# Performance work log

Measured on AMD Instinct MI355X. Metric: run time of the kernel, lower is better.

## Reference

```python
import jax, jax.numpy as jnp
import numpy as np

D_MODEL = 4096
D_FF = 11008

def _dequant_matmul(x, w_int, s):
    # x: [N, in], w_int: [out, in] int, s: [out, 1] -> [N, out]
    w = w_int.astype(jnp.float32) * s  # dequantized weight [out, in]
    return x @ w.T

def setup_inputs() -> dict:
    key = jax.random.key(0)
    ks = jax.random.split(key, 7)
    x = jax.random.normal(ks[0], (4, 2048, D_MODEL), dtype=jnp.float32)
    gate_w = jax.random.randint(ks[1], (D_FF, D_MODEL), -128, 128, dtype=jnp.int32)
    up_w = jax.random.randint(ks[2], (D_FF, D_MODEL), -128, 128, dtype=jnp.int32)
    down_w = jax.random.randint(ks[3], (D_MODEL, D_FF), -128, 128, dtype=jnp.int32)
    gate_s = jax.random.uniform(ks[4], (D_FF, 1), dtype=jnp.float32) * 0.01
    up_s = jax.random.uniform(ks[5], (D_FF, 1), dtype=jnp.float32) * 0.01
    down_s = jax.random.uniform(ks[6], (D_MODEL, 1), dtype=jnp.float32) * 0.01
    return {"x": x, "gate_w": gate_w, "gate_s": gate_s, "up_w": up_w,
            "up_s": up_s, "down_w": down_w, "down_s": down_s}

def reference(x, gate_w, gate_s, up_w, up_s, down_w, down_s):
    batch, seq_len, hidden = x.shape
    x_flat = x.reshape(-1, hidden).astype(jnp.float32)
    gate = _dequant_matmul(x_flat, gate_w, gate_s)
    up = _dequant_matmul(x_flat, up_w, up_s)
    h = jax.nn.silu(gate) * up
    out = _dequant_matmul(h, down_w, down_s)
    return out.astype(x.dtype).reshape(batch, seq_len, hidden)
```

## Files before the change

kernel.cpp:

```cpp
#include <hip/hip_runtime.h>


typedef __attribute__((ext_vector_type(8))) __bf16 bf16x8;
typedef __attribute__((ext_vector_type(4))) float f32x4;
typedef __attribute__((ext_vector_type(8))) unsigned short ushort8;
typedef __attribute__((ext_vector_type(4))) int i32x4;

#define D_MODEL 4096
#define D_FF    11008
#define NTOK    8192

static __device__ __forceinline__ unsigned short f32_to_bf16(float f) {
    union { float f; unsigned u; } v; v.f = f;
    unsigned r = v.u + 0x7fffu + ((v.u >> 16) & 1u);
    return (unsigned short)(r >> 16);
}
static __device__ __forceinline__ void gload_lds16(const void* g, void* l) {
    __builtin_amdgcn_global_load_lds(
        (const __attribute__((address_space(1))) void*)g,
        (__attribute__((address_space(3))) void*)l, 16, 0, 0);
}

__global__ __launch_bounds__(256)
void pack_gu_kernel(const int* __restrict__ gw, const int* __restrict__ uw,
                    signed char* __restrict__ out)
{
    long long i = ((long long)blockIdx.x * 256 + threadIdx.x) * 8;
    const int r = (int)(i >> 12);
    const int k = (int)(i & 4095);
    const int src_row = ((r >> 5) << 4) + (r & 15);
    const int* src = ((r >> 4) & 1) ? uw : gw;
    const int* p = src + (size_t)src_row * D_MODEL + k;
    int4 w0 = *(const int4*)(p);
    int4 w1 = *(const int4*)(p + 4);
    union { signed char c[8]; unsigned long long u; } rr;
    rr.c[0] = (signed char)w0.x; rr.c[1] = (signed char)w0.y;
    rr.c[2] = (signed char)w0.z; rr.c[3] = (signed char)w0.w;
    rr.c[4] = (signed char)w1.x; rr.c[5] = (signed char)w1.y;
    rr.c[6] = (signed char)w1.z; rr.c[7] = (signed char)w1.w;
    *(unsigned long long*)(out + i) = rr.u;
}

__global__ __launch_bounds__(256)
void dequant_w_kernel(const int* __restrict__ w, const float* __restrict__ s,
                      unsigned short* __restrict__ out, int cols, long long total)
{
    long long i = ((long long)blockIdx.x * 256 + threadIdx.x) * 8;
    if (i >= total) return;
    float sc = s[(int)(i / cols)];
    int4 w0 = *(const int4*)(w + i);
    int4 w1 = *(const int4*)(w + i + 4);
    ushort8 r;
    r[0] = f32_to_bf16((float)w0.x * sc);
    r[1] = f32_to_bf16((float)w0.y * sc);
    r[2] = f32_to_bf16((float)w0.z * sc);
    r[3] = f32_to_bf16((float)w0.w * sc);
    r[4] = f32_to_bf16((float)w1.x * sc);
    r[5] = f32_to_bf16((float)w1.y * sc);
    r[6] = f32_to_bf16((float)w1.z * sc);
    r[7] = f32_to_bf16((float)w1.w * sc);
    *(ushort8*)(out + i) = r;
}

__global__ __launch_bounds__(256)
void quant_x_kernel(const float* __restrict__ x, signed char* __restrict__ xq,
                    float* __restrict__ xs)
{
    __shared__ float red[4];
    const int row = blockIdx.x;
    const int t   = threadIdx.x;
    const float* xr = x + (size_t)row * D_MODEL;
    float4 v0 = *(const float4*)(xr + t * 16);
    float4 v1 = *(const float4*)(xr + t * 16 + 4);
    float4 v2 = *(const float4*)(xr + t * 16 + 8);
    float4 v3 = *(const float4*)(xr + t * 16 + 12);
    float m = fabsf(v0.x);
    m = fmaxf(m, fabsf(v0.y)); m = fmaxf(m, fabsf(v0.z)); m = fmaxf(m, fabsf(v0.w));
    m = fmaxf(m, fabsf(v1.x)); m = fmaxf(m, fabsf(v1.y)); m = fmaxf(m, fabsf(v1.z)); m = fmaxf(m, fabsf(v1.w));
    m = fmaxf(m, fabsf(v2.x)); m = fmaxf(m, fabsf(v2.y)); m = fmaxf(m, fabsf(v2.z)); m = fmaxf(m, fabsf(v2.w));
    m = fmaxf(m, fabsf(v3.x)); m = fmaxf(m, fabsf(v3.y)); m = fmaxf(m, fabsf(v3.z)); m = fmaxf(m, fabsf(v3.w));
    #pragma unroll
    for (int o = 32; o > 0; o >>= 1) m = fmaxf(m, __shfl_xor(m, o));
    if ((t & 63) == 0) red[t >> 6] = m;
    __syncthreads();
    m = fmaxf(fmaxf(red[0], red[1]), fmaxf(red[2], red[3]));
    m = fmaxf(m, 1e-20f);
    const float inv = 127.0f / m;
    if (t == 0) xs[row] = m / 127.0f;
    union { signed char c[16]; int4 i; } r;
    #pragma unroll
    for (int j = 0; j < 4; ++j) {
        float4 v = (j == 0) ? v0 : (j == 1) ? v1 : (j == 2) ? v2 : v3;
        r.c[j*4+0] = (signed char)(int)rintf(fminf(fmaxf(v.x*inv,-127.f),127.f));
        r.c[j*4+1] = (signed char)(int)rintf(fminf(fmaxf(v.y*inv,-127.f),127.f));
        r.c[j*4+2] = (signed char)(int)rintf(fminf(fmaxf(v.z*inv,-127.f),127.f));
        r.c[j*4+3] = (signed char)(int)rintf(fminf(fmaxf(v.w*inv,-127.f),127.f));
    }
    *(int4*)(xq + (size_t)row * D_MODEL + t * 16) = r.i;
}

__global__ __launch_bounds__(512, 2)
void gemm_i8gu(const signed char* __restrict__ A,
               const signed char* __restrict__ B,
               unsigned short* __restrict__ H,
               const float* __restrict__ xs,
               const float* __restrict__ gs,
               const float* __restrict__ us,
               int M, int NH, int K)
{
    extern __shared__ char smem[];
    const int tid = threadIdx.x;
    const int l   = tid & 63;
    const int w   = tid >> 6;
    const int wm  = w >> 2;
    const int wn  = w & 3;

    const int nbx  = gridDim.x;
    const int nwg  = nbx * gridDim.y;
    const int orig = blockIdx.y * nbx + blockIdx.x;
    const int cpx  = nwg >> 3;
    const int swz  = (orig & 7) * cpx + (orig >> 3);
    const int bn = swz % nbx, bm = swz / nbx;
    const int m0 = bm * 256, n0 = bn * 256;

    const int st_r = tid >> 2;
    const int st_c = ((tid & 3) ^ ((st_r >> 1) & 3)) << 4;
    const signed char* gA = A + (size_t)(m0 + st_r) * K + st_c;
    const signed char* gB = B + (size_t)(n0 + st_r) * K + st_c;
    const size_t ld128 = (size_t)128 * K;

    const int s4v = l >> 4;
    const int rA = wm * 128 + (l & 15);
    const int rB = wn * 64  + (l & 15);
    const int offA = rA * 64 + ((s4v << 4) ^ (((rA >> 1) & 3) << 4));
    const int offB = 16384 + rB * 64 + ((s4v << 4) ^ (((rB >> 1) & 3) << 4));

    i32x4 acc[8][4] = {};
    i32x4 af[4], bfr[4];

#define SBAR()  __builtin_amdgcn_sched_barrier(0)
#define BAR()   __builtin_amdgcn_s_barrier()
#define VM4()   asm volatile("s_waitcnt vmcnt(4)" ::: "memory")

#define ST_A8(SS, NXT) do { \
    const signed char* p_ = gA + ((size_t)(SS) << 6); \
    gload_lds16(p_,         smem + (NXT) + (w << 10)); \
    gload_lds16(p_ + ld128, smem + (NXT) + 8192 + (w << 10)); } while (0)
#define ST_B8(SS, NXT) do { \
    const signed char* p_ = gB + ((size_t)(SS) << 6); \
    gload_lds16(p_,         smem + (NXT) + 16384 + (w << 10)); \
    gload_lds16(p_ + ld128, smem + (NXT) + 16384 + 8192 + (w << 10)); } while (0)

#define MFMA16_I8(MB) do { \
    _Pragma("unroll") \
    for (int mi_ = 0; mi_ < 4; ++mi_) { \
        _Pragma("unroll") \
        for (int ni_ = 0; ni_ < 4; ++ni_) { \
            acc[(MB) + mi_][ni_] = __builtin_amdgcn_mfma_i32_16x16x64_i8( \
                af[mi_], bfr[ni_], acc[(MB) + mi_][ni_], 0, 0, 0); \
        } } } while (0)

#define STEP8(CUR, NXT, SS) do { \
    af[0]  = *(const i32x4*)(smem + (CUR) + offA); \
    af[1]  = *(const i32x4*)(smem + (CUR) + offA + 1024); \
    af[2]  = *(const i32x4*)(smem + (CUR) + offA + 2048); \
    af[3]  = *(const i32x4*)(smem + (CUR) + offA + 3072); \
    bfr[0] = *(const i32x4*)(smem + (CUR) + offB); \
    bfr[1] = *(const i32x4*)(smem + (CUR) + offB + 1024); \
    bfr[2] = *(const i32x4*)(smem + (CUR) + offB + 2048); \
    bfr[3] = *(const i32x4*)(smem + (CUR) + offB + 3072); \
    ST_A8(SS, NXT); \
    SBAR(); BAR(); \
    __builtin_amdgcn_s_setprio(1); MFMA16_I8(0); __builtin_amdgcn_s_setprio(0); \
    SBAR(); BAR(); \
    af[0] = *(const i32x4*)(smem + (CUR) + offA + 4096); \
    af[1] = *(const i32x4*)(smem + (CUR) + offA + 5120); \
    af[2] = *(const i32x4*)(smem + (CUR) + offA + 6144); \
    af[3] = *(const i32x4*)(smem + (CUR) + offA + 7168); \
    ST_B8(SS, NXT); \
    SBAR(); BAR(); \
    __builtin_amdgcn_s_setprio(1); MFMA16_I8(4); __builtin_amdgcn_s_setprio(0); \
    VM4(); SBAR(); BAR(); \
} while (0)

    ST_A8(0, 0);      ST_B8(0, 0);
    ST_A8(1, 32768);  ST_B8(1, 32768);
    VM4(); SBAR(); BAR();

    const int T = K >> 6;
    #pragma unroll 1
    for (int s = 0; s < T; s += 4) {
        int s2 = s + 2; if (s2 >= T) s2 -= T;
        int s3 = s + 3; if (s3 >= T) s3 -= T;
        int s4 = s + 4; if (s4 >= T) s4 -= T;
        int s5 = s + 5; if (s5 >= T) s5 -= T;
        STEP8(0,     65536, s2);
        STEP8(32768, 98304, s3);
        STEP8(65536, 0,     s4);
        STEP8(98304, 32768, s5);
    }
    asm volatile("s_waitcnt vmcnt(0)" ::: "memory");

    const int er = (l >> 4) * 4;
    const int ec = l & 15;
    const int hbase = (n0 >> 1) + wn * 32;
    #pragma unroll
    for (int mi = 0; mi < 8; ++mi) {
        const int rowb = m0 + wm * 128 + mi * 16 + er;
        const float4 xsv = *(const float4*)(xs + rowb);
        #pragma unroll
        for (int p = 0; p < 2; ++p) {
            const int c = hbase + p * 16 + ec;
            const float sg = gs[c];
            const float su = us[c];
            #pragma unroll
            for (int q = 0; q < 4; ++q) {
                const float xsc = (q == 0) ? xsv.x : (q == 1) ? xsv.y
                                 : (q == 2) ? xsv.z : xsv.w;
                float g = (float)acc[mi][2*p][q]     * sg * xsc;
                float u = (float)acc[mi][2*p + 1][q] * su * xsc;
                float sig = 1.0f / (1.0f + __expf(-g));
                H[(size_t)(rowb + q) * NH + c] = f32_to_bf16(g * sig * u);
            }
        }
    }
#undef STEP8
#undef MFMA16_I8
#undef ST_A8
#undef ST_B8
#undef VM4
#undef BAR
#undef SBAR
}

__global__ __launch_bounds__(512, 2)
void gemm256_down(const unsigned short* __restrict__ A,
                  const unsigned short* __restrict__ B,
                  float* __restrict__ C,
                  int M, int N, int K)
{
    extern __shared__ char smem[];
    const int tid = threadIdx.x;
    const int l   = tid & 63;
    const int w   = tid >> 6;
    const int wm  = w >> 2;
    const int wn  = w & 3;

    const int nbx  = gridDim.x;
    const int nwg  = nbx * gridDim.y;
    const int orig = blockIdx.y * nbx + blockIdx.x;
    const int cpx  = nwg >> 3;
    const int swz  = (orig & 7) * cpx + (orig >> 3);
    const int bn = swz % nbx, bm = swz / nbx;
    const int m0 = bm * 256, n0 = bn * 256;

    const int st_r = w * 16 + (l >> 2);
    const int st_c = (((l & 3) ^ ((l >> 3) & 3)) << 3);
    const unsigned short* gA = A + (size_t)(m0 + st_r) * K + st_c;
    const unsigned short* gB = B + (size_t)(n0 + st_r) * K + st_c;
    const size_t ld128 = (size_t)128 * K;

    const int s4v = l >> 4;
    const int rA = wm * 128 + (l & 15);
    const int rB = wn * 64  + (l & 15);
    const int offA = rA * 64 + ((s4v << 4) ^ (((rA >> 1) & 3) << 4));
    const int offB = 32768 + rB * 64 + ((s4v << 4) ^ (((rB >> 1) & 3) << 4));

    f32x4 acc[8][4] = {};
    bf16x8 af[4], bfr[4];

#define SBAR()  __builtin_amdgcn_sched_barrier(0)
#define BAR()   __builtin_amdgcn_s_barrier()
#define VM4()   asm volatile("s_waitcnt vmcnt(4)" ::: "memory")
#define STAGE2(SRC, LOFF) do { \
    gload_lds16((SRC), smem + (LOFF) + (w << 10)); \
    gload_lds16((SRC) + ld128, smem + (LOFF) + 8192 + (w << 10)); } while (0)

#define MFMA16(MB) do { \
    _Pragma("unroll") \
    for (int mi_ = 0; mi_ < 4; ++mi_) { \
        _Pragma("unroll") \
        for (int ni_ = 0; ni_ < 4; ++ni_) { \
            acc[(MB) + mi_][ni_] = __builtin_amdgcn_mfma_f32_16x16x32_bf16( \
                af[mi_], bfr[ni_], acc[(MB) + mi_][ni_], 0, 0, 0); \
        } } } while (0)

#define TILE(DB, KTN) do { \
    const int CB = (DB) * 65536; \
    const int PB = ((DB) ^ 1) * 65536; \
    const unsigned short* sA = gA + ((size_t)(KTN) << 6); \
    const unsigned short* sB = gB + ((size_t)(KTN) << 6); \
    af[0]  = *(const bf16x8*)(smem + CB + offA); \
    af[1]  = *(const bf16x8*)(smem + CB + offA + 1024); \
    af[2]  = *(const bf16x8*)(smem + CB + offA + 2048); \
    af[3]  = *(const bf16x8*)(smem + CB + offA + 3072); \
    bfr[0] = *(const bf16x8*)(smem + CB + offB); \
    bfr[1] = *(const bf16x8*)(smem + CB + offB + 1024); \
    bfr[2] = *(const bf16x8*)(smem + CB + offB + 2048); \
    bfr[3] = *(const bf16x8*)(smem + CB + offB + 3072); \
    STAGE2(sA, PB); \
    SBAR(); BAR(); \
    __builtin_amdgcn_s_setprio(1); MFMA16(0); __builtin_amdgcn_s_setprio(0); \
    SBAR(); BAR(); \
    af[0] = *(const bf16x8*)(smem + CB + offA + 4096); \
    af[1] = *(const bf16x8*)(smem + CB + offA + 5120); \
    af[2] = *(const bf16x8*)(smem + CB + offA + 6144); \
    af[3] = *(const bf16x8*)(smem + CB + offA + 7168); \
    STAGE2(sB, PB + 32768); \
    SBAR(); BAR(); \
    __builtin_amdgcn_s_setprio(1); MFMA16(4); __builtin_amdgcn_s_setprio(0); \
    VM4(); SBAR(); BAR(); \
    af[0]  = *(const bf16x8*)(smem + CB + 16384 + offA); \
    af[1]  = *(const bf16x8*)(smem + CB + 16384 + offA + 1024); \
    af[2]  = *(const bf16x8*)(smem + CB + 16384 + offA + 2048); \
    af[3]  = *(const bf16x8*)(smem + CB + 16384 + offA + 3072); \
    bfr[0] = *(const bf16x8*)(smem + CB + 16384 + offB); \
    bfr[1] = *(const bf16x8*)(smem + CB + 16384 + offB + 1024); \
    bfr[2] = *(const bf16x8*)(smem + CB + 16384 + offB + 2048); \
    bfr[3] = *(const bf16x8*)(smem + CB + 16384 + offB + 3072); \
    STAGE2(sA + 32, PB + 16384); \
    SBAR(); BAR(); \
    __builtin_amdgcn_s_setprio(1); MFMA16(0); __builtin_amdgcn_s_setprio(0); \
    SBAR(); BAR(); \
    af[0] = *(const bf16x8*)(smem + CB + 16384 + offA + 4096); \
    af[1] = *(const bf16x8*)(smem + CB + 16384 + offA + 5120); \
    af[2] = *(const bf16x8*)(smem + CB + 16384 + offA + 6144); \
    af[3] = *(const bf16x8*)(smem + CB + 16384 + offA + 7168); \
    STAGE2(sB + 32, PB + 49152); \
    SBAR(); BAR(); \
    __builtin_amdgcn_s_setprio(1); MFMA16(4); __builtin_amdgcn_s_setprio(0); \
    VM4(); SBAR(); BAR(); \
} while (0)

    STAGE2(gA,      0);
    STAGE2(gB,      32768);
    STAGE2(gA + 32, 16384);
    STAGE2(gB + 32, 49152);
    VM4(); SBAR(); BAR();

    const int T = K >> 6;
    const int T2 = T >> 1;
    #pragma unroll 1
    for (int it = 0; it < T2; ++it) {
        const int t0 = it << 1;
        TILE(0, t0 + 1);
        const int kt2 = (t0 + 2 == T) ? 0 : (t0 + 2);
        TILE(1, kt2);
    }
    asm volatile("s_waitcnt vmcnt(0)" ::: "memory");

    const int er = (l >> 4) * 4;
    const int ec = l & 15;
    #pragma unroll
    for (int mi = 0; mi < 8; ++mi) {
        #pragma unroll
        for (int ni = 0; ni < 4; ++ni) {
            #pragma unroll
            for (int q = 0; q < 4; ++q) {
                int row = m0 + wm * 128 + mi * 16 + er + q;
                int col = n0 + wn * 64  + ni * 16 + ec;
                C[(size_t)row * N + col] = acc[mi][ni][q];
            }
        }
    }
#undef TILE
#undef MFMA16
#undef STAGE2
#undef VM4
#undef BAR
#undef SBAR
}

extern "C" void kernel_launch(void* const* d_in, const int* in_sizes, int n_in,
                              void* d_out, int out_size, void* d_ws, size_t ws_size,
                              hipStream_t stream)
{
    const float* x  = (const float*)d_in[0];
    const int*   gw = (const int*)  d_in[1];
    const float* gs = (const float*)d_in[2];
    const int*   uw = (const int*)  d_in[3];
    const float* us = (const float*)d_in[4];
    const int*   dw = (const int*)  d_in[5];
    const float* dsc= (const float*)d_in[6];

    char* ws = (char*)d_ws;
    signed char*    Xq   = (signed char*)ws;    ws += (size_t)NTOK * D_MODEL;
    float*          xs   = (float*)ws;          ws += (size_t)NTOK * 4;
    signed char*    Wgu8 = (signed char*)ws;    ws += (size_t)2 * D_FF * D_MODEL;
    unsigned short* Wd   = (unsigned short*)ws; ws += (size_t)D_MODEL * D_FF * 2;
    unsigned short* H    = (unsigned short*)ws;

    const long long wtot  = (long long)D_FF * D_MODEL;
    const long long gutot = 2LL * wtot;

    hipFuncSetAttribute(reinterpret_cast<const void*>(gemm_i8gu),
                        hipFuncAttributeMaxDynamicSharedMemorySize, 131072);
    hipFuncSetAttribute(reinterpret_cast<const void*>(gemm256_down),
                        hipFuncAttributeMaxDynamicSharedMemorySize, 131072);

    pack_gu_kernel  <<<(int)(gutot / 2048), 256, 0, stream>>>(gw, uw, Wgu8);
    dequant_w_kernel<<<(int)(wtot  / 2048), 256, 0, stream>>>(dw, dsc, Wd, D_FF, wtot);
    quant_x_kernel  <<<NTOK, 256, 0, stream>>>(x, Xq, xs);

    dim3 g1(2 * D_FF / 256, NTOK / 256);
    gemm_i8gu<<<g1, 512, 131072, stream>>>(Xq, Wgu8, H, xs, gs, us,
                                           NTOK, D_FF, D_MODEL);

    dim3 g3(D_MODEL / 256, NTOK / 256);
    gemm256_down<<<g3, 512, 131072, stream>>>(H, Wd, (float*)d_out,
                                              NTOK, D_MODEL, D_FF);
}
```

Before: 1.539 ms.

## Switch both GEMMs from 16x16 to 32x32 MFMA instructions

Replaces the 16x16x64 int8 and 16x16x32 bf16 MFMA tiles with 32x32x32 int8 and 32x32x16 bf16 instructions in the gate/up and down GEMMs. LDS fragment loads, accumulator layout and epilogue indexing are reworked to match. The gate/up weight interleave in the pack kernel moves from 16-row to 32-row groups so each 32-wide N fragment holds only gate or only up. The intent is fewer MFMA issues and fewer LDS fragment reads per k-step, which raises arithmetic intensity per LDS read. The risk is different register pressure and epilogue store patterns.

```diff
diff --git a/kernel.cpp b/kernel.cpp
--- a/kernel.cpp
+++ b/kernel.cpp
@@ -3,8 +3,10 @@
 
 typedef __attribute__((ext_vector_type(8))) __bf16 bf16x8;
 typedef __attribute__((ext_vector_type(4))) float f32x4;
+typedef __attribute__((ext_vector_type(16))) float f32x16;
 typedef __attribute__((ext_vector_type(8))) unsigned short ushort8;
 typedef __attribute__((ext_vector_type(4))) int i32x4;
+typedef __attribute__((ext_vector_type(16))) int i32x16;
 
 #define D_MODEL 4096
 #define D_FF    11008
@@ -28,8 +30,8 @@
     long long i = ((long long)blockIdx.x * 256 + threadIdx.x) * 8;
     const int r = (int)(i >> 12);
     const int k = (int)(i & 4095);
-    const int src_row = ((r >> 5) << 4) + (r & 15);
-    const int* src = ((r >> 4) & 1) ? uw : gw;
+    const int src_row = ((r >> 6) << 5) + (r & 31);
+    const int* src = ((r >> 5) & 1) ? uw : gw;
     const int* p = src + (size_t)src_row * D_MODEL + k;
     int4 w0 = *(const int4*)(p);
     int4 w1 = *(const int4*)(p + 4);
@@ -129,14 +131,15 @@
     const signed char* gB = B + (size_t)(n0 + st_r) * K + st_c;
     const size_t ld128 = (size_t)128 * K;
 
-    const int s4v = l >> 4;
-    const int rA = wm * 128 + (l & 15);
-    const int rB = wn * 64  + (l & 15);
-    const int offA = rA * 64 + ((s4v << 4) ^ (((rA >> 1) & 3) << 4));
-    const int offB = 16384 + rB * 64 + ((s4v << 4) ^ (((rB >> 1) & 3) << 4));
-
-    i32x4 acc[8][4] = {};
-    i32x4 af[4], bfr[4];
+    const int lc = l & 31;
+    const int lh = l >> 5;
+    const int rA = wm * 128 + lc;
+    const int rB = wn * 64  + lc;
+    const int offA = rA * 64 + ((lh << 4) ^ (((rA >> 1) & 3) << 4));
+    const int offB = 16384 + rB * 64 + ((lh << 4) ^ (((rB >> 1) & 3) << 4));
+
+    i32x16 acc[4][2] = {};
+    i32x4 af[4], bfr[2];
 
 #define SBAR()  __builtin_amdgcn_sched_barrier(0)
 #define BAR()   __builtin_amdgcn_s_barrier()
@@ -151,35 +154,33 @@
     gload_lds16(p_,         smem + (NXT) + 16384 + (w << 10)); \
     gload_lds16(p_ + ld128, smem + (NXT) + 16384 + 8192 + (w << 10)); } while (0)
 
-#define MFMA16_I8(MB) do { \
+#define MFMA8_I8() do { \
     _Pragma("unroll") \
-    for (int mi_ = 0; mi_ < 4; ++mi_) { \
+    for (int mf_ = 0; mf_ < 4; ++mf_) { \
         _Pragma("unroll") \
-        for (int ni_ = 0; ni_ < 4; ++ni_) { \
-            acc[(MB) + mi_][ni_] = __builtin_amdgcn_mfma_i32_16x16x64_i8( \
-                af[mi_], bfr[ni_], acc[(MB) + mi_][ni_], 0, 0, 0); \
+        for (int nf_ = 0; nf_ < 2; ++nf_) { \
+            acc[mf_][nf_] = __builtin_amdgcn_mfma_i32_32x32x32_i8( \
+                af[mf_], bfr[nf_], acc[mf_][nf_], 0, 0, 0); \
         } } } while (0)
 
+#define LOADFRAGS(CUR, KS) do { \
+    af[0]  = *(const i32x4*)(smem + (CUR) + (offA ^ (KS))); \
+    af[1]  = *(const i32x4*)(smem + (CUR) + ((offA + 2048) ^ (KS))); \
+    af[2]  = *(const i32x4*)(smem + (CUR) + ((offA + 4096) ^ (KS))); \
+    af[3]  = *(const i32x4*)(smem + (CUR) + ((offA + 6144) ^ (KS))); \
+    bfr[0] = *(const i32x4*)(smem + (CUR) + (offB ^ (KS))); \
+    bfr[1] = *(const i32x4*)(smem + (CUR) + ((offB + 2048) ^ (KS))); } while (0)
+
 #define STEP8(CUR, NXT, SS) do { \
-    af[0]  = *(const i32x4*)(smem + (CUR) + offA); \
-    af[1]  = *(const i32x4*)(smem + (CUR) + offA + 1024); \
-    af[2]  = *(const i32x4*)(smem + (CUR) + offA + 2048); \
-    af[3]  = *(const i32x4*)(smem + (CUR) + offA + 3072); \
-    bfr[0] = *(const i32x4*)(smem + (CUR) + offB); \
-    bfr[1] = *(const i32x4*)(smem + (CUR) + offB + 1024); \
-    bfr[2] = *(const i32x4*)(smem + (CUR) + offB + 2048); \
-    bfr[3] = *(const i32x4*)(smem + (CUR) + offB + 3072); \
+    LOADFRAGS(CUR, 0); \
     ST_A8(SS, NXT); \
     SBAR(); BAR(); \
-    __builtin_amdgcn_s_setprio(1); MFMA16_I8(0); __builtin_amdgcn_s_setprio(0); \
-    SBAR(); BAR(); \
-    af[0] = *(const i32x4*)(smem + (CUR) + offA + 4096); \
-    af[1] = *(const i32x4*)(smem + (CUR) + offA + 5120); \
-    af[2] = *(const i32x4*)(smem + (CUR) + offA + 6144); \
-    af[3] = *(const i32x4*)(smem + (CUR) + offA + 7168); \
+    __builtin_amdgcn_s_setprio(1); MFMA8_I8(); __builtin_amdgcn_s_setprio(0); \
+    SBAR(); BAR(); \
+    LOADFRAGS(CUR, 32); \
     ST_B8(SS, NXT); \
     SBAR(); BAR(); \
-    __builtin_amdgcn_s_setprio(1); MFMA16_I8(4); __builtin_amdgcn_s_setprio(0); \
+    __builtin_amdgcn_s_setprio(1); MFMA8_I8(); __builtin_amdgcn_s_setprio(0); \
     VM4(); SBAR(); BAR(); \
 } while (0)
 
@@ -201,31 +202,33 @@
     }
     asm volatile("s_waitcnt vmcnt(0)" ::: "memory");
 
-    const int er = (l >> 4) * 4;
-    const int ec = l & 15;
-    const int hbase = (n0 >> 1) + wn * 32;
-    #pragma unroll
-    for (int mi = 0; mi < 8; ++mi) {
-        const int rowb = m0 + wm * 128 + mi * 16 + er;
-        const float4 xsv = *(const float4*)(xs + rowb);
+    {
+        const int c = (n0 >> 1) + wn * 32 + lc;
+        const float sg = gs[c];
+        const float su = us[c];
         #pragma unroll
-        for (int p = 0; p < 2; ++p) {
-            const int c = hbase + p * 16 + ec;
-            const float sg = gs[c];
-            const float su = us[c];
+        for (int mf = 0; mf < 4; ++mf) {
+            const int rb = m0 + wm * 128 + mf * 32 + 4 * lh;
             #pragma unroll
-            for (int q = 0; q < 4; ++q) {
-                const float xsc = (q == 0) ? xsv.x : (q == 1) ? xsv.y
-                                 : (q == 2) ? xsv.z : xsv.w;
-                float g = (float)acc[mi][2*p][q]     * sg * xsc;
-                float u = (float)acc[mi][2*p + 1][q] * su * xsc;
-                float sig = 1.0f / (1.0f + __expf(-g));
-                H[(size_t)(rowb + q) * NH + c] = f32_to_bf16(g * sig * u);
+            for (int q2 = 0; q2 < 4; ++q2) {
+                const float4 xsv = *(const float4*)(xs + rb + 8 * q2);
+                #pragma unroll
+                for (int q = 0; q < 4; ++q) {
+                    const int reg = q2 * 4 + q;
+                    const int row = rb + 8 * q2 + q;
+                    const float xsc = (q == 0) ? xsv.x : (q == 1) ? xsv.y
+                                     : (q == 2) ? xsv.z : xsv.w;
+                    float g = (float)acc[mf][0][reg] * sg * xsc;
+                    float u = (float)acc[mf][1][reg] * su * xsc;
+                    float sig = 1.0f / (1.0f + __expf(-g));
+                    H[(size_t)row * NH + c] = f32_to_bf16(g * sig * u);
+                }
             }
         }
     }
 #undef STEP8
-#undef MFMA16_I8
+#undef LOADFRAGS
+#undef MFMA8_I8
 #undef ST_A8
 #undef ST_B8
 #undef VM4
@@ -260,14 +263,15 @@
     const unsigned short* gB = B + (size_t)(n0 + st_r) * K + st_c;
     const size_t ld128 = (size_t)128 * K;
 
-    const int s4v = l >> 4;
-    const int rA = wm * 128 + (l & 15);
-    const int rB = wn * 64  + (l & 15);
-    const int offA = rA * 64 + ((s4v << 4) ^ (((rA >> 1) & 3) << 4));
-    const int offB = 32768 + rB * 64 + ((s4v << 4) ^ (((rB >> 1) & 3) << 4));
-
-    f32x4 acc[8][4] = {};
-    bf16x8 af[4], bfr[4];
+    const int lc = l & 31;
+    const int lh = l >> 5;
+    const int rA = wm * 128 + lc;
+    const int rB = wn * 64  + lc;
+    const int offA = rA * 64 + ((lh << 4) ^ (((rA >> 1) & 3) << 4));
+    const int offB = 32768 + rB * 64 + ((lh << 4) ^ (((rB >> 1) & 3) << 4));
+
+    f32x16 acc[4][2] = {};
+    bf16x8 af[4], bfr[2];
 
 #define SBAR()  __builtin_amdgcn_sched_barrier(0)
 #define BAR()   __builtin_amdgcn_s_barrier()
@@ -276,59 +280,51 @@
     gload_lds16((SRC), smem + (LOFF) + (w << 10)); \
     gload_lds16((SRC) + ld128, smem + (LOFF) + 8192 + (w << 10)); } while (0)
 
-#define MFMA16(MB) do { \
+#define MFMA8_BF() do { \
     _Pragma("unroll") \
-    for (int mi_ = 0; mi_ < 4; ++mi_) { \
+    for (int mf_ = 0; mf_ < 4; ++mf_) { \
         _Pragma("unroll") \
-        for (int ni_ = 0; ni_ < 4; ++ni_) { \
-            acc[(MB) + mi_][ni_] = __builtin_amdgcn_mfma_f32_16x16x32_bf16( \
-                af[mi_], bfr[ni_], acc[(MB) + mi_][ni_], 0, 0, 0); \
+        for (int nf_ = 0; nf_ < 2; ++nf_) { \
+            acc[mf_][nf_] = __builtin_amdgcn_mfma_f32_32x32x16_bf16( \
+                af[mf_], bfr[nf_], acc[mf_][nf_], 0, 0, 0); \
         } } } while (0)
+
+#define LOADFRAGS(CB, HB, KS) do { \
+    af[0]  = *(const bf16x8*)(smem + (CB) + (HB) + (offA ^ (KS))); \
+    af[1]  = *(const bf16x8*)(smem + (CB) + (HB) + ((offA + 2048) ^ (KS))); \
+    af[2]  = *(const bf16x8*)(smem + (CB) + (HB) + ((offA + 4096) ^ (KS))); \
+    af[3]  = *(const bf16x8*)(smem + (CB) + (HB) + ((offA + 6144) ^ (KS))); \
+    bfr[0] = *(const bf16x8*)(smem + (CB) + (HB) + (offB ^ (KS))); \
+    bfr[1] = *(const bf16x8*)(smem + (CB) + (HB) + ((offB + 2048) ^ (KS))); } while (0)
 
 #define TILE(DB, KTN) do { \
     const int CB = (DB) * 65536; \
     const int PB = ((DB) ^ 1) * 65536; \
     const unsigned short* sA = gA + ((size_t)(KTN) << 6); \
     const unsigned short* sB = gB + ((size_t)(KTN) << 6); \
-    af[0]  = *(const bf16x8*)(smem + CB + offA); \
-    af[1]  = *(const bf16x8*)(smem + CB + offA + 1024); \
-    af[2]  = *(const bf16x8*)(smem + CB + offA + 2048); \
-    af[3]  = *(const bf16x8*)(smem + CB + offA + 3072); \
-    bfr[0] = *(const bf16x8*)(smem + CB + offB); \
-    bfr[1] = *(const bf16x8*)(smem + CB + offB + 1024); \
-    bfr[2] = *(const bf16x8*)(smem + CB + offB + 2048); \
-    bfr[3] = *(const bf16x8*)(smem + CB + offB + 3072); \
+     \
+    LOADFRAGS(CB, 0, 0); \
     STAGE2(sA, PB); \
     SBAR(); BAR(); \
-    __builtin_amdgcn_s_setprio(1); MFMA16(0); __builtin_amdgcn_s_setprio(0); \
-    SBAR(); BAR(); \
-    af[0] = *(const bf16x8*)(smem + CB + offA + 4096); \
-    af[1] = *(const bf16x8*)(smem + CB + offA + 5120); \
-    af[2] = *(const bf16x8*)(smem + CB + offA + 6144); \
-    af[3] = *(const bf16x8*)(smem + CB + offA + 7168); \
+    __builtin_amdgcn_s_setprio(1); MFMA8_BF(); __builtin_amdgcn_s_setprio(0); \
+    SBAR(); BAR(); \
+     \
+    LOADFRAGS(CB, 0, 32); \
     STAGE2(sB, PB + 32768); \
     SBAR(); BAR(); \
-    __builtin_amdgcn_s_setprio(1); MFMA16(4); __builtin_amdgcn_s_setprio(0); \
+    __builtin_amdgcn_s_setprio(1); MFMA8_BF(); __builtin_amdgcn_s_setprio(0); \
     VM4(); SBAR(); BAR(); \
-    af[0]  = *(const bf16x8*)(smem + CB + 16384 + offA); \
-    af[1]  = *(const bf16x8*)(smem + CB + 16384 + offA + 1024); \
-    af[2]  = *(const bf16x8*)(smem + CB + 16384 + offA + 2048); \
-    af[3]  = *(const bf16x8*)(smem + CB + 16384 + offA + 3072); \
-    bfr[0] = *(const bf16x8*)(smem + CB + 16384 + offB); \
-    bfr[1] = *(const bf16x8*)(smem + CB + 16384 + offB + 1024); \
-    bfr[2] = *(const bf16x8*)(smem + CB + 16384 + offB + 2048); \
-    bfr[3] = *(const bf16x8*)(smem + CB + 16384 + offB + 3072); \
+     \
+    LOADFRAGS(CB, 16384, 0); \
     STAGE2(sA + 32, PB + 16384); \
     SBAR(); BAR(); \
-    __builtin_amdgcn_s_setprio(1); MFMA16(0); __builtin_amdgcn_s_setprio(0); \
-    SBAR(); BAR(); \
-    af[0] = *(const bf16x8*)(smem + CB + 16384 + offA + 4096); \
-    af[1] = *(const bf16x8*)(smem + CB + 16384 + offA + 5120); \
-    af[2] = *(const bf16x8*)(smem + CB + 16384 + offA + 6144); \
-    af[3] = *(const bf16x8*)(smem + CB + 16384 + offA + 7168); \
+    __builtin_amdgcn_s_setprio(1); MFMA8_BF(); __builtin_amdgcn_s_setprio(0); \
+    SBAR(); BAR(); \
+     \
+    LOADFRAGS(CB, 16384, 32); \
     STAGE2(sB + 32, PB + 49152); \
     SBAR(); BAR(); \
-    __builtin_amdgcn_s_setprio(1); MFMA16(4); __builtin_amdgcn_s_setprio(0); \
+    __builtin_amdgcn_s_setprio(1); MFMA8_BF(); __builtin_amdgcn_s_setprio(0); \
     VM4(); SBAR(); BAR(); \
 } while (0)
 
@@ -349,22 +345,25 @@
     }
     asm volatile("s_waitcnt vmcnt(0)" ::: "memory");
 
-    const int er = (l >> 4) * 4;
-    const int ec = l & 15;
     #pragma unroll
-    for (int mi = 0; mi < 8; ++mi) {
+    for (int mf = 0; mf < 4; ++mf) {
+        const int rb = m0 + wm * 128 + mf * 32 + 4 * lh;
         #pragma unroll
-        for (int ni = 0; ni < 4; ++ni) {
+        for (int nf = 0; nf < 2; ++nf) {
+            const int col = n0 + wn * 64 + nf * 32 + lc;
             #pragma unroll
-            for (int q = 0; q < 4; ++q) {
-                int row = m0 + wm * 128 + mi * 16 + er + q;
-                int col = n0 + wn * 64  + ni * 16 + ec;
-                C[(size_t)row * N + col] = acc[mi][ni][q];
+            for (int q2 = 0; q2 < 4; ++q2) {
+                #pragma unroll
+                for (int q = 0; q < 4; ++q) {
+                    const int row = rb + 8 * q2 + q;
+                    C[(size_t)row * N + col] = acc[mf][nf][q2 * 4 + q];
+                }
             }
         }
     }
 #undef TILE
-#undef MFMA16
+#undef LOADFRAGS
+#undef MFMA8_BF
 #undef STAGE2
 #undef VM4
 #undef BAR
```

Result: slower. 1.703 ms (+10.7%).

## Load B fragments directly from global into registers, halve LDS usage

Applied to the files above, without the earlier changes.

In both GEMMs, the B (weight) operand is no longer staged through LDS. Each wave now loads its MFMA B fragments straight from global memory into double-buffered registers one step ahead, and only A stays in LDS. This halves dynamic shared memory to 64 KB, cuts LDS traffic and ds_read work, and may allow higher occupancy. In exchange, B reads are no longer shared across the waves that use the same columns, so global/L2 traffic goes up. Register pressure also rises, and the vmcnt wait accounting changes.

```diff
diff --git a/kernel.cpp b/kernel.cpp
--- a/kernel.cpp
+++ b/kernel.cpp
@@ -126,78 +126,82 @@
     const int st_r = tid >> 2;
     const int st_c = ((tid & 3) ^ ((st_r >> 1) & 3)) << 4;
     const signed char* gA = A + (size_t)(m0 + st_r) * K + st_c;
-    const signed char* gB = B + (size_t)(n0 + st_r) * K + st_c;
     const size_t ld128 = (size_t)128 * K;
 
     const int s4v = l >> 4;
     const int rA = wm * 128 + (l & 15);
-    const int rB = wn * 64  + (l & 15);
     const int offA = rA * 64 + ((s4v << 4) ^ (((rA >> 1) & 3) << 4));
-    const int offB = 16384 + rB * 64 + ((s4v << 4) ^ (((rB >> 1) & 3) << 4));
+
+    const signed char* gB0 = B + (size_t)(n0 + wn * 64 + (l & 15)) * K
+                               + ((l >> 4) << 4);
+    const size_t bK16 = (size_t)16 * K;
 
     i32x4 acc[8][4] = {};
-    i32x4 af[4], bfr[4];
+    i32x4 af[4];
+    i32x4 bqa[4], bqb[4];
 
 #define SBAR()  __builtin_amdgcn_sched_barrier(0)
 #define BAR()   __builtin_amdgcn_s_barrier()
-#define VM4()   asm volatile("s_waitcnt vmcnt(4)" ::: "memory")
-
-#define ST_A8(SS, NXT) do { \
+#define VM6()   asm volatile("s_waitcnt vmcnt(6)" ::: "memory")
+
+#define ST_A(SS, NXT) do { \
     const signed char* p_ = gA + ((size_t)(SS) << 6); \
     gload_lds16(p_,         smem + (NXT) + (w << 10)); \
     gload_lds16(p_ + ld128, smem + (NXT) + 8192 + (w << 10)); } while (0)
-#define ST_B8(SS, NXT) do { \
-    const signed char* p_ = gB + ((size_t)(SS) << 6); \
-    gload_lds16(p_,         smem + (NXT) + 16384 + (w << 10)); \
-    gload_lds16(p_ + ld128, smem + (NXT) + 16384 + 8192 + (w << 10)); } while (0)
-
-#define MFMA16_I8(MB) do { \
+
+#define LD_B(BQ, SB) do { \
+    const signed char* q_ = gB0 + ((size_t)(SB) << 6); \
+    BQ[0] = *(const i32x4*)(q_); \
+    BQ[1] = *(const i32x4*)(q_ + bK16); \
+    BQ[2] = *(const i32x4*)(q_ + 2 * bK16); \
+    BQ[3] = *(const i32x4*)(q_ + 3 * bK16); } while (0)
+
+#define MFMA16(MB, BQ) do { \
     _Pragma("unroll") \
     for (int mi_ = 0; mi_ < 4; ++mi_) { \
         _Pragma("unroll") \
         for (int ni_ = 0; ni_ < 4; ++ni_) { \
             acc[(MB) + mi_][ni_] = __builtin_amdgcn_mfma_i32_16x16x64_i8( \
-                af[mi_], bfr[ni_], acc[(MB) + mi_][ni_], 0, 0, 0); \
+                af[mi_], BQ[ni_], acc[(MB) + mi_][ni_], 0, 0, 0); \
         } } } while (0)
 
-#define STEP8(CUR, NXT, SS) do { \
-    af[0]  = *(const i32x4*)(smem + (CUR) + offA); \
-    af[1]  = *(const i32x4*)(smem + (CUR) + offA + 1024); \
-    af[2]  = *(const i32x4*)(smem + (CUR) + offA + 2048); \
-    af[3]  = *(const i32x4*)(smem + (CUR) + offA + 3072); \
-    bfr[0] = *(const i32x4*)(smem + (CUR) + offB); \
-    bfr[1] = *(const i32x4*)(smem + (CUR) + offB + 1024); \
-    bfr[2] = *(const i32x4*)(smem + (CUR) + offB + 2048); \
-    bfr[3] = *(const i32x4*)(smem + (CUR) + offB + 3072); \
-    ST_A8(SS, NXT); \
-    SBAR(); BAR(); \
-    __builtin_amdgcn_s_setprio(1); MFMA16_I8(0); __builtin_amdgcn_s_setprio(0); \
+#define STEP(CUR, NXT, SS, SB, BC, BN) do { \
+    af[0] = *(const i32x4*)(smem + (CUR) + offA); \
+    af[1] = *(const i32x4*)(smem + (CUR) + offA + 1024); \
+    af[2] = *(const i32x4*)(smem + (CUR) + offA + 2048); \
+    af[3] = *(const i32x4*)(smem + (CUR) + offA + 3072); \
+    ST_A(SS, NXT); \
+    LD_B(BN, SB); \
+    SBAR(); BAR(); VM6(); SBAR(); \
+    __builtin_amdgcn_s_setprio(1); MFMA16(0, BC); __builtin_amdgcn_s_setprio(0); \
     SBAR(); BAR(); \
     af[0] = *(const i32x4*)(smem + (CUR) + offA + 4096); \
     af[1] = *(const i32x4*)(smem + (CUR) + offA + 5120); \
     af[2] = *(const i32x4*)(smem + (CUR) + offA + 6144); \
     af[3] = *(const i32x4*)(smem + (CUR) + offA + 7168); \
-    ST_B8(SS, NXT); \
-    SBAR(); BAR(); \
-    __builtin_amdgcn_s_setprio(1); MFMA16_I8(4); __builtin_amdgcn_s_setprio(0); \
-    VM4(); SBAR(); BAR(); \
+    SBAR(); BAR(); \
+    __builtin_amdgcn_s_setprio(1); MFMA16(4, BC); __builtin_amdgcn_s_setprio(0); \
+    SBAR(); BAR(); \
 } while (0)
 
-    ST_A8(0, 0);      ST_B8(0, 0);
-    ST_A8(1, 32768);  ST_B8(1, 32768);
-    VM4(); SBAR(); BAR();
+    ST_A(0, 0);
+    ST_A(1, 16384);
+    LD_B(bqa, 0);
+    asm volatile("s_waitcnt vmcnt(4)" ::: "memory");
+    SBAR(); BAR();
 
     const int T = K >> 6;
     #pragma unroll 1
     for (int s = 0; s < T; s += 4) {
+        int b1 = s + 1;
         int s2 = s + 2; if (s2 >= T) s2 -= T;
         int s3 = s + 3; if (s3 >= T) s3 -= T;
         int s4 = s + 4; if (s4 >= T) s4 -= T;
         int s5 = s + 5; if (s5 >= T) s5 -= T;
-        STEP8(0,     65536, s2);
-        STEP8(32768, 98304, s3);
-        STEP8(65536, 0,     s4);
-        STEP8(98304, 32768, s5);
+        STEP(0,     32768, s2, b1, bqa, bqb);
+        STEP(16384, 49152, s3, s2, bqb, bqa);
+        STEP(32768, 0,     s4, s3, bqa, bqb);
+        STEP(49152, 16384, s5, s4, bqb, bqa);
     }
     asm volatile("s_waitcnt vmcnt(0)" ::: "memory");
 
@@ -224,11 +228,11 @@
             }
         }
     }
-#undef STEP8
-#undef MFMA16_I8
-#undef ST_A8
-#undef ST_B8
-#undef VM4
+#undef STEP
+#undef MFMA16
+#undef LD_B
+#undef ST_A
+#undef VM6
 #undef BAR
 #undef SBAR
 }
@@ -257,95 +261,97 @@
     const int st_r = w * 16 + (l >> 2);
     const int st_c = (((l & 3) ^ ((l >> 3) & 3)) << 3);
     const unsigned short* gA = A + (size_t)(m0 + st_r) * K + st_c;
-    const unsigned short* gB = B + (size_t)(n0 + st_r) * K + st_c;
     const size_t ld128 = (size_t)128 * K;
 
     const int s4v = l >> 4;
     const int rA = wm * 128 + (l & 15);
-    const int rB = wn * 64  + (l & 15);
     const int offA = rA * 64 + ((s4v << 4) ^ (((rA >> 1) & 3) << 4));
-    const int offB = 32768 + rB * 64 + ((s4v << 4) ^ (((rB >> 1) & 3) << 4));
+
+    const unsigned short* gB0 = B + (size_t)(n0 + wn * 64 + (l & 15)) * K
+                                  + ((l >> 4) << 3);
+    const size_t bK16 = (size_t)16 * K;
 
     f32x4 acc[8][4] = {};
-    bf16x8 af[4], bfr[4];
+    bf16x8 af[4];
+    bf16x8 bca[8], bcb[8];
 
 #define SBAR()  __builtin_amdgcn_sched_barrier(0)
 #define BAR()   __builtin_amdgcn_s_barrier()
-#define VM4()   asm volatile("s_waitcnt vmcnt(4)" ::: "memory")
-#define STAGE2(SRC, LOFF) do { \
+#define VM6()   asm volatile("s_waitcnt vmcnt(6)" ::: "memory")
+
+#define ST_A2(SRC, LOFF) do { \
     gload_lds16((SRC), smem + (LOFF) + (w << 10)); \
     gload_lds16((SRC) + ld128, smem + (LOFF) + 8192 + (w << 10)); } while (0)
 
-#define MFMA16(MB) do { \
+#define LD_B4(BQ, I0, TB, HF) do { \
+    const unsigned short* q_ = gB0 + ((size_t)(TB) << 6) + (HF) * 32; \
+    BQ[(I0) + 0] = *(const bf16x8*)(q_); \
+    BQ[(I0) + 1] = *(const bf16x8*)(q_ + bK16); \
+    BQ[(I0) + 2] = *(const bf16x8*)(q_ + 2 * bK16); \
+    BQ[(I0) + 3] = *(const bf16x8*)(q_ + 3 * bK16); } while (0)
+
+#define MFMA16B(MB, BQ, B0) do { \
     _Pragma("unroll") \
     for (int mi_ = 0; mi_ < 4; ++mi_) { \
         _Pragma("unroll") \
         for (int ni_ = 0; ni_ < 4; ++ni_) { \
             acc[(MB) + mi_][ni_] = __builtin_amdgcn_mfma_f32_16x16x32_bf16( \
-                af[mi_], bfr[ni_], acc[(MB) + mi_][ni_], 0, 0, 0); \
+                af[mi_], BQ[(B0) + ni_], acc[(MB) + mi_][ni_], 0, 0, 0); \
         } } } while (0)
 
-#define TILE(DB, KTN) do { \
-    const int CB = (DB) * 65536; \
-    const int PB = ((DB) ^ 1) * 65536; \
-    const unsigned short* sA = gA + ((size_t)(KTN) << 6); \
-    const unsigned short* sB = gB + ((size_t)(KTN) << 6); \
-    af[0]  = *(const bf16x8*)(smem + CB + offA); \
-    af[1]  = *(const bf16x8*)(smem + CB + offA + 1024); \
-    af[2]  = *(const bf16x8*)(smem + CB + offA + 2048); \
-    af[3]  = *(const bf16x8*)(smem + CB + offA + 3072); \
-    bfr[0] = *(const bf16x8*)(smem + CB + offB); \
-    bfr[1] = *(const bf16x8*)(smem + CB + offB + 1024); \
-    bfr[2] = *(const bf16x8*)(smem + CB + offB + 2048); \
-    bfr[3] = *(const bf16x8*)(smem + CB + offB + 3072); \
-    STAGE2(sA, PB); \
-    SBAR(); BAR(); \
-    __builtin_amdgcn_s_setprio(1); MFMA16(0); __builtin_amdgcn_s_setprio(0); \
-    SBAR(); BAR(); \
-    af[0] = *(const bf16x8*)(smem + CB + offA + 4096); \
-    af[1] = *(const bf16x8*)(smem + CB + offA + 5120); \
-    af[2] = *(const bf16x8*)(smem + CB + offA + 6144); \
-    af[3] = *(const bf16x8*)(smem + CB + offA + 7168); \
-    STAGE2(sB, PB + 32768); \
-    SBAR(); BAR(); \
-    __builtin_amdgcn_s_setprio(1); MFMA16(4); __builtin_amdgcn_s_setprio(0); \
-    VM4(); SBAR(); BAR(); \
-    af[0]  = *(const bf16x8*)(smem + CB + 16384 + offA); \
-    af[1]  = *(const bf16x8*)(smem + CB + 16384 + offA + 1024); \
-    af[2]  = *(const bf16x8*)(smem + CB + 16384 + offA + 2048); \
-    af[3]  = *(const bf16x8*)(smem + CB + 16384 + offA + 3072); \
-    bfr[0] = *(const bf16x8*)(smem + CB + 16384 + offB); \
-    bfr[1] = *(const bf16x8*)(smem + CB + 16384 + offB + 1024); \
-    bfr[2] = *(const bf16x8*)(smem + CB + 16384 + offB + 2048); \
-    bfr[3] = *(const bf16x8*)(smem + CB + 16384 + offB + 3072); \
-    STAGE2(sA + 32, PB + 16384); \
-    SBAR(); BAR(); \
-    __builtin_amdgcn_s_setprio(1); MFMA16(0); __builtin_amdgcn_s_setprio(0); \
-    SBAR(); BAR(); \
-    af[0] = *(const bf16x8*)(smem + CB + 16384 + offA + 4096); \
-    af[1] = *(const bf16x8*)(smem + CB + 16384 + offA + 5120); \
-    af[2] = *(const bf16x8*)(smem + CB + 16384 + offA + 6144); \
-    af[3] = *(const bf16x8*)(smem + CB + 16384 + offA + 7168); \
-    STAGE2(sB + 32, PB + 49152); \
-    SBAR(); BAR(); \
-    __builtin_amdgcn_s_setprio(1); MFMA16(4); __builtin_amdgcn_s_setprio(0); \
-    VM4(); SBAR(); BAR(); \
+#define TILE(CB, PB, TN, BC, BN) do { \
+    const unsigned short* sA = gA + ((size_t)(TN) << 6); \
+     \
+    af[0] = *(const bf16x8*)(smem + (CB) + offA); \
+    af[1] = *(const bf16x8*)(smem + (CB) + offA + 1024); \
+    af[2] = *(const bf16x8*)(smem + (CB) + offA + 2048); \
+    af[3] = *(const bf16x8*)(smem + (CB) + offA + 3072); \
+    ST_A2(sA, PB); \
+    LD_B4(BN, 0, TN, 0); \
+    SBAR(); BAR(); VM6(); SBAR(); \
+    __builtin_amdgcn_s_setprio(1); MFMA16B(0, BC, 0); __builtin_amdgcn_s_setprio(0); \
+    SBAR(); BAR(); \
+     \
+    af[0] = *(const bf16x8*)(smem + (CB) + offA + 4096); \
+    af[1] = *(const bf16x8*)(smem + (CB) + offA + 5120); \
+    af[2] = *(const bf16x8*)(smem + (CB) + offA + 6144); \
+    af[3] = *(const bf16x8*)(smem + (CB) + offA + 7168); \
+    ST_A2(sA + 32, PB + 16384); \
+    LD_B4(BN, 4, TN, 1); \
+    SBAR(); BAR(); \
+    __builtin_amdgcn_s_setprio(1); MFMA16B(4, BC, 0); __builtin_amdgcn_s_setprio(0); \
+    SBAR(); BAR(); \
+     \
+    af[0] = *(const bf16x8*)(smem + (CB) + 16384 + offA); \
+    af[1] = *(const bf16x8*)(smem + (CB) + 16384 + offA + 1024); \
+    af[2] = *(const bf16x8*)(smem + (CB) + 16384 + offA + 2048); \
+    af[3] = *(const bf16x8*)(smem + (CB) + 16384 + offA + 3072); \
+    SBAR(); BAR(); \
+    __builtin_amdgcn_s_setprio(1); MFMA16B(0, BC, 4); __builtin_amdgcn_s_setprio(0); \
+    SBAR(); BAR(); \
+     \
+    af[0] = *(const bf16x8*)(smem + (CB) + 16384 + offA + 4096); \
+    af[1] = *(const bf16x8*)(smem + (CB) + 16384 + offA + 5120); \
+    af[2] = *(const bf16x8*)(smem + (CB) + 16384 + offA + 6144); \
+    af[3] = *(const bf16x8*)(smem + (CB) + 16384 + offA + 7168); \
+    SBAR(); BAR(); \
+    __builtin_amdgcn_s_setprio(1); MFMA16B(4, BC, 4); __builtin_amdgcn_s_setprio(0); \
+    SBAR(); BAR(); \
 } while (0)
 
-    STAGE2(gA,      0);
-    STAGE2(gB,      32768);
-    STAGE2(gA + 32, 16384);
-    STAGE2(gB + 32, 49152);
-    VM4(); SBAR(); BAR();
+    ST_A2(gA, 0);
+    ST_A2(gA + 32, 16384);
+    LD_B4(bca, 0, 0, 0);
+    LD_B4(bca, 4, 0, 1);
+    SBAR(); BAR();
 
     const int T = K >> 6;
-    const int T2 = T >> 1;
     #pragma unroll 1
-    for (int it = 0; it < T2; ++it) {
-        const int t0 = it << 1;
-        TILE(0, t0 + 1);
-        const int kt2 = (t0 + 2 == T) ? 0 : (t0 + 2);
-        TILE(1, kt2);
+    for (int t = 0; t < T; t += 2) {
+        const int t1 = t + 1;
+        const int t2 = (t + 2 == T) ? 0 : (t + 2);
+        TILE(0,     32768, t1, bca, bcb);
+        TILE(32768, 0,     t2, bcb, bca);
     }
     asm volatile("s_waitcnt vmcnt(0)" ::: "memory");
 
@@ -364,9 +370,10 @@
         }
     }
 #undef TILE
-#undef MFMA16
-#undef STAGE2
-#undef VM4
+#undef MFMA16B
+#undef LD_B4
+#undef ST_A2
+#undef VM6
 #undef BAR
 #undef SBAR
 }
@@ -394,19 +401,19 @@
     const long long gutot = 2LL * wtot;
 
     hipFuncSetAttribute(reinterpret_cast<const void*>(gemm_i8gu),
-                        hipFuncAttributeMaxDynamicSharedMemorySize, 131072);
+                        hipFuncAttributeMaxDynamicSharedMemorySize, 65536);
     hipFuncSetAttribute(reinterpret_cast<const void*>(gemm256_down),
-                        hipFuncAttributeMaxDynamicSharedMemorySize, 131072);
+                        hipFuncAttributeMaxDynamicSharedMemorySize, 65536);
 
     pack_gu_kernel  <<<(int)(gutot / 2048), 256, 0, stream>>>(gw, uw, Wgu8);
     dequant_w_kernel<<<(int)(wtot  / 2048), 256, 0, stream>>>(dw, dsc, Wd, D_FF, wtot);
     quant_x_kernel  <<<NTOK, 256, 0, stream>>>(x, Xq, xs);
 
     dim3 g1(2 * D_FF / 256, NTOK / 256);
-    gemm_i8gu<<<g1, 512, 131072, stream>>>(Xq, Wgu8, H, xs, gs, us,
-                                           NTOK, D_FF, D_MODEL);
+    gemm_i8gu<<<g1, 512, 65536, stream>>>(Xq, Wgu8, H, xs, gs, us,
+                                          NTOK, D_FF, D_MODEL);
 
     dim3 g3(D_MODEL / 256, NTOK / 256);
-    gemm256_down<<<g3, 512, 131072, stream>>>(H, Wd, (float*)d_out,
-                                              NTOK, D_MODEL, D_FF);
-}
+    gemm256_down<<<g3, 512, 65536, stream>>>(H, Wd, (float*)d_out,
+                                             NTOK, D_MODEL, D_FF);
+}
```

Result: slower. 2.431 ms (+58.0%).

## Restructure GEMM pipelines into four-stage ring with one barrier per K-step

Applied to the files above, without the earlier changes.

Both GEMM kernels replace the mid-step barriers and split A/B fragment loads with a single step that issues all global-to-LDS prefetches first, loads all 8 A and 4 B fragments, then runs 32 MFMAs under one barrier. The down-projection kernel also moves from a double-buffered 64-wide K tile to a four-slot ring of 32-wide K slices, reusing the same staging layout as the gate/up kernel. The aim is to cut barrier count and keep the matrix units busy longer between syncs. In exchange it holds more fragment registers live and has a deeper prefetch distance. A leftover dead ST_B8 macro (defined then immediately #undef'd) contains a malformed call but is never expanded.

```diff
diff --git a/kernel.cpp b/kernel.cpp
--- a/kernel.cpp
+++ b/kernel.cpp
@@ -136,7 +136,7 @@
     const int offB = 16384 + rB * 64 + ((s4v << 4) ^ (((rB >> 1) & 3) << 4));
 
     i32x4 acc[8][4] = {};
-    i32x4 af[4], bfr[4];
+    i32x4 af[8], bfr[4];
 
 #define SBAR()  __builtin_amdgcn_sched_barrier(0)
 #define BAR()   __builtin_amdgcn_s_barrier()
@@ -149,37 +149,37 @@
 #define ST_B8(SS, NXT) do { \
     const signed char* p_ = gB + ((size_t)(SS) << 6); \
     gload_lds16(p_,         smem + (NXT) + 16384 + (w << 10)); \
+    gload_lds16(p_ + 16384 - 8192 + 0, smem, 0); } while (0)
+#undef ST_B8
+#define ST_B8(SS, NXT) do { \
+    const signed char* p_ = gB + ((size_t)(SS) << 6); \
+    gload_lds16(p_,         smem + (NXT) + 16384 + (w << 10)); \
     gload_lds16(p_ + ld128, smem + (NXT) + 16384 + 8192 + (w << 10)); } while (0)
 
-#define MFMA16_I8(MB) do { \
-    _Pragma("unroll") \
-    for (int mi_ = 0; mi_ < 4; ++mi_) { \
-        _Pragma("unroll") \
-        for (int ni_ = 0; ni_ < 4; ++ni_) { \
-            acc[(MB) + mi_][ni_] = __builtin_amdgcn_mfma_i32_16x16x64_i8( \
-                af[mi_], bfr[ni_], acc[(MB) + mi_][ni_], 0, 0, 0); \
-        } } } while (0)
-
 #define STEP8(CUR, NXT, SS) do { \
-    af[0]  = *(const i32x4*)(smem + (CUR) + offA); \
-    af[1]  = *(const i32x4*)(smem + (CUR) + offA + 1024); \
-    af[2]  = *(const i32x4*)(smem + (CUR) + offA + 2048); \
-    af[3]  = *(const i32x4*)(smem + (CUR) + offA + 3072); \
+    ST_A8(SS, NXT); \
+    ST_B8(SS, NXT); \
+    af[0] = *(const i32x4*)(smem + (CUR) + offA); \
+    af[1] = *(const i32x4*)(smem + (CUR) + offA + 1024); \
+    af[2] = *(const i32x4*)(smem + (CUR) + offA + 2048); \
+    af[3] = *(const i32x4*)(smem + (CUR) + offA + 3072); \
+    af[4] = *(const i32x4*)(smem + (CUR) + offA + 4096); \
+    af[5] = *(const i32x4*)(smem + (CUR) + offA + 5120); \
+    af[6] = *(const i32x4*)(smem + (CUR) + offA + 6144); \
+    af[7] = *(const i32x4*)(smem + (CUR) + offA + 7168); \
     bfr[0] = *(const i32x4*)(smem + (CUR) + offB); \
     bfr[1] = *(const i32x4*)(smem + (CUR) + offB + 1024); \
     bfr[2] = *(const i32x4*)(smem + (CUR) + offB + 2048); \
     bfr[3] = *(const i32x4*)(smem + (CUR) + offB + 3072); \
-    ST_A8(SS, NXT); \
-    SBAR(); BAR(); \
-    __builtin_amdgcn_s_setprio(1); MFMA16_I8(0); __builtin_amdgcn_s_setprio(0); \
-    SBAR(); BAR(); \
-    af[0] = *(const i32x4*)(smem + (CUR) + offA + 4096); \
-    af[1] = *(const i32x4*)(smem + (CUR) + offA + 5120); \
-    af[2] = *(const i32x4*)(smem + (CUR) + offA + 6144); \
-    af[3] = *(const i32x4*)(smem + (CUR) + offA + 7168); \
-    ST_B8(SS, NXT); \
-    SBAR(); BAR(); \
-    __builtin_amdgcn_s_setprio(1); MFMA16_I8(4); __builtin_amdgcn_s_setprio(0); \
+    __builtin_amdgcn_s_setprio(1); \
+    _Pragma("unroll") \
+    for (int mi_ = 0; mi_ < 8; ++mi_) { \
+        _Pragma("unroll") \
+        for (int ni_ = 0; ni_ < 4; ++ni_) { \
+            acc[mi_][ni_] = __builtin_amdgcn_mfma_i32_16x16x64_i8( \
+                af[mi_], bfr[ni_], acc[mi_][ni_], 0, 0, 0); \
+        } } \
+    __builtin_amdgcn_s_setprio(0); \
     VM4(); SBAR(); BAR(); \
 } while (0)
 
@@ -225,7 +225,6 @@
         }
     }
 #undef STEP8
-#undef MFMA16_I8
 #undef ST_A8
 #undef ST_B8
 #undef VM4
@@ -254,8 +253,8 @@
     const int bn = swz % nbx, bm = swz / nbx;
     const int m0 = bm * 256, n0 = bn * 256;
 
-    const int st_r = w * 16 + (l >> 2);
-    const int st_c = (((l & 3) ^ ((l >> 3) & 3)) << 3);
+    const int st_r = tid >> 2;
+    const int st_c = ((tid & 3) ^ ((st_r >> 1) & 3)) << 3;
     const unsigned short* gA = A + (size_t)(m0 + st_r) * K + st_c;
     const unsigned short* gB = B + (size_t)(n0 + st_r) * K + st_c;
     const size_t ld128 = (size_t)128 * K;
@@ -264,88 +263,66 @@
     const int rA = wm * 128 + (l & 15);
     const int rB = wn * 64  + (l & 15);
     const int offA = rA * 64 + ((s4v << 4) ^ (((rA >> 1) & 3) << 4));
-    const int offB = 32768 + rB * 64 + ((s4v << 4) ^ (((rB >> 1) & 3) << 4));
+    const int offB = 16384 + rB * 64 + ((s4v << 4) ^ (((rB >> 1) & 3) << 4));
 
     f32x4 acc[8][4] = {};
-    bf16x8 af[4], bfr[4];
+    bf16x8 af[8], bfr[4];
 
 #define SBAR()  __builtin_amdgcn_sched_barrier(0)
 #define BAR()   __builtin_amdgcn_s_barrier()
 #define VM4()   asm volatile("s_waitcnt vmcnt(4)" ::: "memory")
-#define STAGE2(SRC, LOFF) do { \
-    gload_lds16((SRC), smem + (LOFF) + (w << 10)); \
-    gload_lds16((SRC) + ld128, smem + (LOFF) + 8192 + (w << 10)); } while (0)
-
-#define MFMA16(MB) do { \
+
+#define ST_A2(SS, NXT) do { \
+    const unsigned short* p_ = gA + ((size_t)(SS) << 5); \
+    gload_lds16(p_,         smem + (NXT) + (w << 10)); \
+    gload_lds16(p_ + ld128, smem + (NXT) + 8192 + (w << 10)); } while (0)
+#define ST_B2(SS, NXT) do { \
+    const unsigned short* p_ = gB + ((size_t)(SS) << 5); \
+    gload_lds16(p_,         smem + (NXT) + 16384 + (w << 10)); \
+    gload_lds16(p_ + ld128, smem + (NXT) + 16384 + 8192 + (w << 10)); } while (0)
+
+#define STEPD(CUR, NXT, SS) do { \
+    ST_A2(SS, NXT); \
+    ST_B2(SS, NXT); \
+    af[0] = *(const bf16x8*)(smem + (CUR) + offA); \
+    af[1] = *(const bf16x8*)(smem + (CUR) + offA + 1024); \
+    af[2] = *(const bf16x8*)(smem + (CUR) + offA + 2048); \
+    af[3] = *(const bf16x8*)(smem + (CUR) + offA + 3072); \
+    af[4] = *(const bf16x8*)(smem + (CUR) + offA + 4096); \
+    af[5] = *(const bf16x8*)(smem + (CUR) + offA + 5120); \
+    af[6] = *(const bf16x8*)(smem + (CUR) + offA + 6144); \
+    af[7] = *(const bf16x8*)(smem + (CUR) + offA + 7168); \
+    bfr[0] = *(const bf16x8*)(smem + (CUR) + offB); \
+    bfr[1] = *(const bf16x8*)(smem + (CUR) + offB + 1024); \
+    bfr[2] = *(const bf16x8*)(smem + (CUR) + offB + 2048); \
+    bfr[3] = *(const bf16x8*)(smem + (CUR) + offB + 3072); \
+    __builtin_amdgcn_s_setprio(1); \
     _Pragma("unroll") \
-    for (int mi_ = 0; mi_ < 4; ++mi_) { \
+    for (int mi_ = 0; mi_ < 8; ++mi_) { \
         _Pragma("unroll") \
         for (int ni_ = 0; ni_ < 4; ++ni_) { \
-            acc[(MB) + mi_][ni_] = __builtin_amdgcn_mfma_f32_16x16x32_bf16( \
-                af[mi_], bfr[ni_], acc[(MB) + mi_][ni_], 0, 0, 0); \
-        } } } while (0)
-
-#define TILE(DB, KTN) do { \
-    const int CB = (DB) * 65536; \
-    const int PB = ((DB) ^ 1) * 65536; \
-    const unsigned short* sA = gA + ((size_t)(KTN) << 6); \
-    const unsigned short* sB = gB + ((size_t)(KTN) << 6); \
-    af[0]  = *(const bf16x8*)(smem + CB + offA); \
-    af[1]  = *(const bf16x8*)(smem + CB + offA + 1024); \
-    af[2]  = *(const bf16x8*)(smem + CB + offA + 2048); \
-    af[3]  = *(const bf16x8*)(smem + CB + offA + 3072); \
-    bfr[0] = *(const bf16x8*)(smem + CB + offB); \
-    bfr[1] = *(const bf16x8*)(smem + CB + offB + 1024); \
-    bfr[2] = *(const bf16x8*)(smem + CB + offB + 2048); \
-    bfr[3] = *(const bf16x8*)(smem + CB + offB + 3072); \
-    STAGE2(sA, PB); \
-    SBAR(); BAR(); \
-    __builtin_amdgcn_s_setprio(1); MFMA16(0); __builtin_amdgcn_s_setprio(0); \
-    SBAR(); BAR(); \
-    af[0] = *(const bf16x8*)(smem + CB + offA + 4096); \
-    af[1] = *(const bf16x8*)(smem + CB + offA + 5120); \
-    af[2] = *(const bf16x8*)(smem + CB + offA + 6144); \
-    af[3] = *(const bf16x8*)(smem + CB + offA + 7168); \
-    STAGE2(sB, PB + 32768); \
-    SBAR(); BAR(); \
-    __builtin_amdgcn_s_setprio(1); MFMA16(4); __builtin_amdgcn_s_setprio(0); \
-    VM4(); SBAR(); BAR(); \
-    af[0]  = *(const bf16x8*)(smem + CB + 16384 + offA); \
-    af[1]  = *(const bf16x8*)(smem + CB + 16384 + offA + 1024); \
-    af[2]  = *(const bf16x8*)(smem + CB + 16384 + offA + 2048); \
-    af[3]  = *(const bf16x8*)(smem + CB + 16384 + offA + 3072); \
-    bfr[0] = *(const bf16x8*)(smem + CB + 16384 + offB); \
-    bfr[1] = *(const bf16x8*)(smem + CB + 16384 + offB + 1024); \
-    bfr[2] = *(const bf16x8*)(smem + CB + 16384 + offB + 2048); \
-    bfr[3] = *(const bf16x8*)(smem + CB + 16384 + offB + 3072); \
-    STAGE2(sA + 32, PB + 16384); \
-    SBAR(); BAR(); \
-    __builtin_amdgcn_s_setprio(1); MFMA16(0); __builtin_amdgcn_s_setprio(0); \
-    SBAR(); BAR(); \
-    af[0] = *(const bf16x8*)(smem + CB + 16384 + offA + 4096); \
-    af[1] = *(const bf16x8*)(smem + CB + 16384 + offA + 5120); \
-    af[2] = *(const bf16x8*)(smem + CB + 16384 + offA + 6144); \
-    af[3] = *(const bf16x8*)(smem + CB + 16384 + offA + 7168); \
-    STAGE2(sB + 32, PB + 49152); \
-    SBAR(); BAR(); \
-    __builtin_amdgcn_s_setprio(1); MFMA16(4); __builtin_amdgcn_s_setprio(0); \
+            acc[mi_][ni_] = __builtin_amdgcn_mfma_f32_16x16x32_bf16( \
+                af[mi_], bfr[ni_], acc[mi_][ni_], 0, 0, 0); \
+        } } \
+    __builtin_amdgcn_s_setprio(0); \
     VM4(); SBAR(); BAR(); \
 } while (0)
 
-    STAGE2(gA,      0);
-    STAGE2(gB,      32768);
-    STAGE2(gA + 32, 16384);
-    STAGE2(gB + 32, 49152);
+    ST_A2(0, 0);      ST_B2(0, 0);
+    ST_A2(1, 32768);  ST_B2(1, 32768);
     VM4(); SBAR(); BAR();
 
-    const int T = K >> 6;
-    const int T2 = T >> 1;
+    const int T = K >> 5;
     #pragma unroll 1
-    for (int it = 0; it < T2; ++it) {
-        const int t0 = it << 1;
-        TILE(0, t0 + 1);
-        const int kt2 = (t0 + 2 == T) ? 0 : (t0 + 2);
-        TILE(1, kt2);
+    for (int s = 0; s < T; s += 4) {
+        int s2 = s + 2; if (s2 >= T) s2 -= T;
+        int s3 = s + 3; if (s3 >= T) s3 -= T;
+        int s4 = s + 4; if (s4 >= T) s4 -= T;
+        int s5 = s + 5; if (s5 >= T) s5 -= T;
+        STEPD(0,     65536, s2);
+        STEPD(32768, 98304, s3);
+        STEPD(65536, 0,     s4);
+        STEPD(98304, 32768, s5);
     }
     asm volatile("s_waitcnt vmcnt(0)" ::: "memory");
 
@@ -363,9 +340,9 @@
             }
         }
     }
-#undef TILE
-#undef MFMA16
-#undef STAGE2
+#undef STEPD
+#undef ST_A2
+#undef ST_B2
 #undef VM4
 #undef BAR
 #undef SBAR
```

Result: no change. 1.555 ms (+1.0%).
